# Kernel tuning notes

Hardware: AMD Instinct MI355X
Metric: run time of the kernel (lower is better)

Reference implementation:

```python
import jax, jax.numpy as jnp
import numpy as np

N_NODES = 100000
N_EDGES = 1600000
IN_DIM, HID_DIM, OUT_DIM = 128, 64, 64


def setup_inputs() -> dict:
    key = jax.random.key(0)
    ks = jax.random.split(key, 7)
    x = jax.random.normal(ks[0], (N_NODES, IN_DIM), dtype=jnp.float32)
    edge_index = jax.random.randint(ks[1], (2, N_EDGES), 0, N_NODES, dtype=jnp.int64)
    user_idx = jax.random.randint(ks[2], (N_NODES,), 0, N_NODES, dtype=jnp.int64)
    W1 = jax.random.normal(ks[3], (IN_DIM, HID_DIM), dtype=jnp.float32) * (1.0 / np.sqrt(IN_DIM))
    b1 = jax.random.normal(ks[4], (HID_DIM,), dtype=jnp.float32) * 0.02
    W2 = jax.random.normal(ks[5], (HID_DIM, OUT_DIM), dtype=jnp.float32) * (1.0 / np.sqrt(HID_DIM))
    b2 = jax.random.normal(ks[6], (OUT_DIM,), dtype=jnp.float32) * 0.02
    return {"x": x, "edge_index": edge_index, "user_idx": user_idx,
            "W1": W1, "b1": b1, "W2": W2, "b2": b2}


def _gcn_conv(x, edge_index, W, b):
    # PyG GCNConv: linear transform, add self-loops, sym-normalized aggregation.
    N = x.shape[0]
    h = x @ W  # [N, F_out]
    loop = jnp.arange(N, dtype=edge_index.dtype)
    src = jnp.concatenate([edge_index[0], loop])  # [E+N]
    dst = jnp.concatenate([edge_index[1], loop])
    deg = jax.ops.segment_sum(jnp.ones(src.shape[0], dtype=h.dtype), dst, num_segments=N)
    dis = jnp.where(deg > 0, jax.lax.rsqrt(jnp.maximum(deg, 1.0)), 0.0)  # deg^{-1/2}
    norm = dis[src] * dis[dst]  # [E+N]
    msg = h[src] * norm[:, None]  # gather + scale
    out = jax.ops.segment_sum(msg, dst, num_segments=N)  # scatter-add at targets
    return out + b


def _scatter_mean(x, idx, dim_size):
    s = jax.ops.segment_sum(x, idx, num_segments=dim_size)
    cnt = jax.ops.segment_sum(jnp.ones(x.shape[0], dtype=x.dtype), idx, num_segments=dim_size)
    return jnp.where(cnt[:, None] > 0, s / jnp.maximum(cnt[:, None], 1.0), 0.0)


def reference(x, edge_index, user_idx, W1, b1, W2, b2):
    h = _gcn_conv(x, edge_index, W1, b1)
    h = jax.nn.relu(h)
    # dropout is identity in eval mode
    h = _gcn_conv(h, edge_index, W2, b2)
    return _scatter_mean(h, user_idx, h.shape[0])
```

## Files before the change

### kernel.cpp

```cpp
#include <hip/hip_runtime.h>
#include <hip/hip_bf16.h>


#define FEAT 64
#define INDIM 128

#define SCAN_BS 256
#define SCAN_ELEMS 8
#define SCAN_CHUNK (SCAN_BS * SCAN_ELEMS)

#define BIN_SHIFT 9
#define BIN_R 512
#define BIN_TILE 2048
#define BH_TILE 2048

typedef __attribute__((ext_vector_type(8))) short short8;
typedef __attribute__((ext_vector_type(4))) float f32x4;

__device__ __forceinline__ unsigned short f2bf(float f) {
    unsigned u = __float_as_uint(f);
    unsigned r = u + 0x7FFFu + ((u >> 16) & 1u);
    return (unsigned short)(r >> 16);
}
__device__ __forceinline__ float bf2f(unsigned short v) {
    return __uint_as_float(((unsigned)v) << 16);
}


__global__ __launch_bounds__(256) void k_bhist(const int* __restrict__ dst,
                                               int* __restrict__ gbc,
                                               const int* __restrict__ uidx,
                                               float* __restrict__ cntf,
                                               uint4* __restrict__ outz, long nz4,
                                               int E, int N, int KB) {
    __shared__ int h[256];
    const int tid = threadIdx.x;
    h[tid] = 0;
    __syncthreads();
    const int base = blockIdx.x * BH_TILE;
    #pragma unroll
    for (int t = 0; t < BH_TILE / 256; ++t) {
        int e = base + t * 256 + tid;
        if (e < E) {
            int d = dst[e];
            if ((unsigned)d < (unsigned)N) atomicAdd(&h[d >> BIN_SHIFT], 1);
        }
    }
    int i = blockIdx.x * 256 + tid;
    if (i < N) {
        int u = uidx[i];
        if ((unsigned)u < (unsigned)N) atomicAdd(&cntf[u], 1.0f);
    }
    if (outz) {
        uint4 z; z.x = 0; z.y = 0; z.z = 0; z.w = 0;
        const long stride = (long)gridDim.x * 256;
        for (long idx = (long)blockIdx.x * 256 + tid; idx < nz4; idx += stride)
            outz[idx] = z;
    }
    __syncthreads();
    if (tid < KB && h[tid]) atomicAdd(&gbc[tid], h[tid]);
}

__global__ __launch_bounds__(256) void k_bscan(const int* __restrict__ gbc,
                                               int* __restrict__ bb,
                                               int* __restrict__ bcur,
                                               int* __restrict__ rpN, int KB) {
    __shared__ int lds[256];
    const int tid = threadIdx.x;
    int v = (tid < KB) ? gbc[tid] : 0;
    lds[tid] = v;
    __syncthreads();
    for (int d = 1; d < 256; d <<= 1) {
        int t = (tid >= d) ? lds[tid - d] : 0;
        __syncthreads();
        lds[tid] += t;
        __syncthreads();
    }
    int excl = lds[tid] - v;
    if (tid < KB) { bb[tid] = excl; bcur[tid] = excl; }
    if (tid == 255) { bb[KB] = lds[255]; *rpN = lds[255]; }
}

__global__ __launch_bounds__(256) void k_binA(const int* __restrict__ src,
                                              const int* __restrict__ dst,
                                              int* __restrict__ bcur,
                                              unsigned* __restrict__ pairs,
                                              int E, int N, int KB) {
    __shared__ unsigned lbuf[BIN_TILE];
    __shared__ unsigned short bkt[BIN_TILE];
    __shared__ int lcnt[256];
    __shared__ int loff[256];
    __shared__ int lbase[256];
    __shared__ int tot;
    const int tid = threadIdx.x;
    const int base = blockIdx.x * BIN_TILE;

    lcnt[tid] = 0;
    __syncthreads();

    int mys[BIN_TILE / 256], myd[BIN_TILE / 256], myb[BIN_TILE / 256];
    #pragma unroll
    for (int t = 0; t < BIN_TILE / 256; ++t) {
        int e = base + t * 256 + tid;
        int s = 0, d = -1;
        if (e < E) { s = src[e]; d = dst[e]; }
        if ((unsigned)d >= (unsigned)N) d = -1;
        if ((unsigned)s >= (unsigned)N) s = 0;
        mys[t] = s; myd[t] = d;
        myb[t] = (d >= 0) ? (d >> BIN_SHIFT) : -1;
        if (myb[t] >= 0) atomicAdd(&lcnt[myb[t]], 1);
    }
    __syncthreads();

    int v = lcnt[tid];
    loff[tid] = v;
    __syncthreads();
    for (int d = 1; d < 256; d <<= 1) {
        int t2 = (tid >= d) ? loff[tid - d] : 0;
        __syncthreads();
        loff[tid] += t2;
        __syncthreads();
    }
    if (tid == 255) tot = loff[255];
    int excl = loff[tid] - v;
    __syncthreads();
    loff[tid] = excl;
    lcnt[tid] = excl;
    if (tid < KB && v > 0) lbase[tid] = atomicAdd(&bcur[tid], v);
    __syncthreads();

    #pragma unroll
    for (int t = 0; t < BIN_TILE / 256; ++t) {
        if (myb[t] >= 0) {
            int pos = atomicAdd(&lcnt[myb[t]], 1);
            lbuf[pos] = ((unsigned)mys[t] << BIN_SHIFT) | (unsigned)(myd[t] & (BIN_R - 1));
            bkt[pos] = (unsigned short)myb[t];
        }
    }
    __syncthreads();

    const int T = tot;
    for (int i = tid; i < T; i += 256) {
        int b = bkt[i];
        pairs[lbase[b] + (i - loff[b])] = lbuf[i];
    }
}

__global__ __launch_bounds__(1024) void k_binB2(const unsigned* __restrict__ pairs,
                                                const int* __restrict__ bb,
                                                int* __restrict__ rp,
                                                int* __restrict__ col,
                                                float* __restrict__ dis, int N) {
    __shared__ int cnt[BIN_R];
    __shared__ int cur[BIN_R];
    __shared__ int ssum[256];
    const int tid = threadIdx.x;
    const int b = blockIdx.x;
    const int n0 = b << BIN_SHIFT;
    const int n1 = min(n0 + BIN_R, N);
    const int nn = n1 - n0;
    const int e0 = bb[b];
    const int e1 = bb[b + 1];

    for (int i = tid; i < nn; i += 1024) cnt[i] = 0;
    __syncthreads();
    for (int i = e0 + tid; i < e1; i += 1024) {
        atomicAdd(&cnt[pairs[i] & (BIN_R - 1)], 1);
    }
    __syncthreads();

    const int i0 = 2 * tid;
    int c0 = 0, c1 = 0;
    if (tid < 256) {
        c0 = (i0     < nn) ? cnt[i0]     : 0;
        c1 = (i0 + 1 < nn) ? cnt[i0 + 1] : 0;
        ssum[tid] = c0 + c1;
    }
    __syncthreads();
    for (int d = 1; d < 256; d <<= 1) {
        int t = 0;
        if (tid < 256 && tid >= d) t = ssum[tid - d];
        __syncthreads();
        if (tid < 256) ssum[tid] += t;
        __syncthreads();
    }
    if (tid < 256) {
        int excl = ssum[tid] - (c0 + c1);
        if (i0 < nn) {
            cur[i0] = e0 + excl;
            rp[n0 + i0] = e0 + excl;
            dis[n0 + i0] = rsqrtf((float)c0 + 1.0f);
        }
        if (i0 + 1 < nn) {
            cur[i0 + 1] = e0 + excl + c0;
            rp[n0 + i0 + 1] = e0 + excl + c0;
            dis[n0 + i0 + 1] = rsqrtf((float)c1 + 1.0f);
        }
    }
    __syncthreads();

    for (int i = e0 + tid; i < e1; i += 1024) {
        unsigned p = pairs[i];
        int pos = atomicAdd(&cur[p & (BIN_R - 1)], 1);
        col[pos] = (int)(p >> BIN_SHIFT);
    }
}


__global__ __launch_bounds__(256) void k_hist(const int* __restrict__ dst,
                                              int* __restrict__ cntE, int E, int N) {
    int e = blockIdx.x * 256 + threadIdx.x;
    if (e < E) {
        int d = dst[e];
        if ((unsigned)d < (unsigned)N) atomicAdd(&cntE[d], 1);
    }
}
__global__ __launch_bounds__(256) void k_dis(const int* __restrict__ cntE,
                                             float* __restrict__ dis, int N) {
    int i = blockIdx.x * 256 + threadIdx.x;
    if (i < N) dis[i] = rsqrtf((float)cntE[i] + 1.0f);
}
__global__ __launch_bounds__(SCAN_BS) void k_scan1(const int* __restrict__ c,
                                                   int* __restrict__ rp,
                                                   int* __restrict__ ptot, int N) {
    __shared__ int lds[SCAN_BS];
    const int base = blockIdx.x * SCAN_CHUNK;
    const int tb = base + threadIdx.x * SCAN_ELEMS;
    int vals[SCAN_ELEMS];
    int s = 0;
    #pragma unroll
    for (int k = 0; k < SCAN_ELEMS; ++k) {
        int idx = tb + k;
        int v = (idx < N) ? c[idx] : 0;
        vals[k] = s;
        s += v;
    }
    lds[threadIdx.x] = s;
    __syncthreads();
    for (int d = 1; d < SCAN_BS; d <<= 1) {
        int v = (threadIdx.x >= d) ? lds[threadIdx.x - d] : 0;
        __syncthreads();
        lds[threadIdx.x] += v;
        __syncthreads();
    }
    int toff = (threadIdx.x == 0) ? 0 : lds[threadIdx.x - 1];
    #pragma unroll
    for (int k = 0; k < SCAN_ELEMS; ++k) {
        int idx = tb + k;
        if (idx < N) rp[idx] = toff + vals[k];
    }
    if (threadIdx.x == SCAN_BS - 1) ptot[blockIdx.x] = lds[SCAN_BS - 1];
}
__global__ __launch_bounds__(1024) void k_scan2(int* __restrict__ ptot,
                                                int* __restrict__ poff,
                                                int* __restrict__ rpN, int nb) {
    __shared__ int lds[1024];
    int tid = threadIdx.x;
    lds[tid] = (tid < nb) ? ptot[tid] : 0;
    __syncthreads();
    for (int d = 1; d < 1024; d <<= 1) {
        int v = (tid >= d) ? lds[tid - d] : 0;
        __syncthreads();
        lds[tid] += v;
        __syncthreads();
    }
    if (tid < nb) poff[tid] = (tid == 0) ? 0 : lds[tid - 1];
    if (tid == nb - 1) *rpN = lds[tid];
}
__global__ __launch_bounds__(SCAN_BS) void k_scan3(int* __restrict__ rp,
                                                   const int* __restrict__ poff, int N) {
    int off = poff[blockIdx.x];
    const int tb = blockIdx.x * SCAN_CHUNK + threadIdx.x * SCAN_ELEMS;
    #pragma unroll
    for (int k = 0; k < SCAN_ELEMS; ++k) {
        int idx = tb + k;
        if (idx < N) rp[idx] += off;
    }
}
__global__ __launch_bounds__(256) void k_fill(const int* __restrict__ src,
                                              const int* __restrict__ dst,
                                              const int* __restrict__ rp,
                                              int* __restrict__ tmp,
                                              int* __restrict__ col, int E, int N) {
    int e = blockIdx.x * 256 + threadIdx.x;
    if (e >= E) return;
    int s = src[e], d = dst[e];
    if ((unsigned)s >= (unsigned)N) s = 0;
    if ((unsigned)d >= (unsigned)N) return;
    int r = atomicAdd(&tmp[d], 1);
    col[rp[d] + r] = s;
}

__global__ __launch_bounds__(256) void k_ucnt(const int* __restrict__ uidx,
                                              float* __restrict__ cntf, int N) {
    int i = blockIdx.x * 256 + threadIdx.x;
    if (i < N) {
        int u = uidx[i];
        if ((unsigned)u < (unsigned)N) atomicAdd(&cntf[u], 1.0f);
    }
}


__global__ __launch_bounds__(256) void k_gemm1(const float* __restrict__ x,
                                               const float* __restrict__ W,
                                               const float* __restrict__ scale,
                                               unsigned short* __restrict__ out, int N) {
    __shared__ short wf[4 * 4 * 64 * 8];
    const int tid = threadIdx.x;
    if (blockIdx.x == 0 && tid < 8) {
        uint4 z; z.x = 0; z.y = 0; z.z = 0; z.w = 0;
        *reinterpret_cast<uint4*>(out + (long)N * FEAT + tid * 8) = z;
    }
    for (int i = tid; i < INDIM * FEAT; i += 256) {
        int k = i >> 6, n = i & 63;
        int ct = n >> 4, kc = k >> 5, r = k & 31;
        int owner = ((r >> 3) << 4) | (n & 15);
        wf[(((ct << 2) | kc) * 64 + owner) * 8 + (r & 7)] = (short)f2bf(W[i]);
    }
    __syncthreads();

    const int lane = tid & 63;
    const int m = lane & 15, q = lane >> 4;
    const int row0 = blockIdx.x * 64 + (tid >> 6) * 16;

    short8 bfr[4][4];
    #pragma unroll
    for (int ct = 0; ct < 4; ++ct)
        #pragma unroll
        for (int kc = 0; kc < 4; ++kc)
            bfr[ct][kc] = *reinterpret_cast<const short8*>(&wf[(((ct << 2) | kc) * 64 + lane) * 8]);

    int gr = row0 + m;
    int rl = gr < N ? gr : (N - 1);
    const float* xp = x + (long)rl * INDIM + q * 8;

    f32x4 acc[4] = {{0,0,0,0},{0,0,0,0},{0,0,0,0},{0,0,0,0}};
    #pragma unroll
    for (int kc = 0; kc < 4; ++kc) {
        float4 v0 = *reinterpret_cast<const float4*>(xp + kc * 32);
        float4 v1 = *reinterpret_cast<const float4*>(xp + kc * 32 + 4);
        short8 a;
        a[0]=(short)f2bf(v0.x); a[1]=(short)f2bf(v0.y); a[2]=(short)f2bf(v0.z); a[3]=(short)f2bf(v0.w);
        a[4]=(short)f2bf(v1.x); a[5]=(short)f2bf(v1.y); a[6]=(short)f2bf(v1.z); a[7]=(short)f2bf(v1.w);
        #pragma unroll
        for (int ct = 0; ct < 4; ++ct)
            acc[ct] = __builtin_amdgcn_mfma_f32_16x16x32_bf16(a, bfr[ct][kc], acc[ct], 0, 0, 0);
    }

    #pragma unroll
    for (int reg = 0; reg < 4; ++reg) {
        int row = row0 + q * 4 + reg;
        if (row < N) {
            float sc = scale[row];
            #pragma unroll
            for (int ct = 0; ct < 4; ++ct)
                out[(long)row * FEAT + ct * 16 + m] = f2bf(acc[ct][reg] * sc);
        }
    }
}

__global__ __launch_bounds__(256) void k_gemm2(const unsigned short* __restrict__ h,
                                               const float* __restrict__ W,
                                               const float* __restrict__ scale,
                                               unsigned short* __restrict__ out, int N) {
    __shared__ short wf[4 * 2 * 64 * 8];
    const int tid = threadIdx.x;
    if (blockIdx.x == 0 && tid < 8) {
        uint4 z; z.x = 0; z.y = 0; z.z = 0; z.w = 0;
        *reinterpret_cast<uint4*>(out + (long)N * FEAT + tid * 8) = z;
    }
    for (int i = tid; i < FEAT * FEAT; i += 256) {
        int k = i >> 6, n = i & 63;
        int ct = n >> 4, kc = k >> 5, r = k & 31;
        int owner = ((r >> 3) << 4) | (n & 15);
        wf[(((ct << 1) | kc) * 64 + owner) * 8 + (r & 7)] = (short)f2bf(W[i]);
    }
    __syncthreads();

    const int lane = tid & 63;
    const int m = lane & 15, q = lane >> 4;
    const int row0 = blockIdx.x * 64 + (tid >> 6) * 16;

    short8 bfr[4][2];
    #pragma unroll
    for (int ct = 0; ct < 4; ++ct)
        #pragma unroll
        for (int kc = 0; kc < 2; ++kc)
            bfr[ct][kc] = *reinterpret_cast<const short8*>(&wf[(((ct << 1) | kc) * 64 + lane) * 8]);

    int gr = row0 + m;
    int rl = gr < N ? gr : (N - 1);
    const unsigned short* hp = h + (long)rl * FEAT + q * 8;

    f32x4 acc[4] = {{0,0,0,0},{0,0,0,0},{0,0,0,0},{0,0,0,0}};
    #pragma unroll
    for (int kc = 0; kc < 2; ++kc) {
        short8 a = *reinterpret_cast<const short8*>(hp + kc * 32);
        #pragma unroll
        for (int ct = 0; ct < 4; ++ct)
            acc[ct] = __builtin_amdgcn_mfma_f32_16x16x32_bf16(a, bfr[ct][kc], acc[ct], 0, 0, 0);
    }

    #pragma unroll
    for (int reg = 0; reg < 4; ++reg) {
        int row = row0 + q * 4 + reg;
        if (row < N) {
            float sc = scale[row];
            #pragma unroll
            for (int ct = 0; ct < 4; ++ct)
                out[(long)row * FEAT + ct * 16 + m] = f2bf(acc[ct][reg] * sc);
        }
    }
}


#define ACC8(r)                                                                  \
    a0 += bf2f((unsigned short)(r).x);                                           \
    a1 += bf2f((unsigned short)((r).x >> 16));                                   \
    a2 += bf2f((unsigned short)(r).y);                                           \
    a3 += bf2f((unsigned short)((r).y >> 16));                                   \
    a4 += bf2f((unsigned short)(r).z);                                           \
    a5 += bf2f((unsigned short)((r).z >> 16));                                   \
    a6 += bf2f((unsigned short)(r).w);                                           \
    a7 += bf2f((unsigned short)((r).w >> 16));

#define AGG_BODY(SELF_INIT)                                                      \
    const int lane = threadIdx.x & 63;                                           \
    const int wv = threadIdx.x >> 6;                                             \
    const int p  = lane >> 4;                                                    \
    const int s  = (lane >> 3) & 1;                                              \
    const int ol = lane & 7;                                                     \
    const int i  = blockIdx.x * 16 + wv * 4 + p;                                 \
    const bool valid = (i < N);                                                  \
    const int jb = valid ? rp[i] : 0;                                            \
    const int je = valid ? rp[i + 1] : 0;                                        \
    float a0=0.f,a1=0.f,a2=0.f,a3=0.f,a4=0.f,a5=0.f,a6=0.f,a7=0.f;               \
    if (valid && s == 0) { SELF_INIT }                                           \
    for (int j0 = jb; j0 < je; j0 += 16) {                                       \
        int j1 = j0 + s;                                                         \
        int c1 = (j1      < je) ? col[j1]      : N;                              \
        int c2 = (j1 + 2  < je) ? col[j1 + 2]  : N;                              \
        int c3 = (j1 + 4  < je) ? col[j1 + 4]  : N;                              \
        int c4 = (j1 + 6  < je) ? col[j1 + 6]  : N;                              \
        int c5 = (j1 + 8  < je) ? col[j1 + 8]  : N;                              \
        int c6 = (j1 + 10 < je) ? col[j1 + 10] : N;                              \
        int c7 = (j1 + 12 < je) ? col[j1 + 12] : N;                              \
        int c8 = (j1 + 14 < je) ? col[j1 + 14] : N;                              \
        uint4 r1 = *reinterpret_cast<const uint4*>(A + (long)c1 * FEAT + 8 * ol);\
        uint4 r2 = *reinterpret_cast<const uint4*>(A + (long)c2 * FEAT + 8 * ol);\
        uint4 r3 = *reinterpret_cast<const uint4*>(A + (long)c3 * FEAT + 8 * ol);\
        uint4 r4 = *reinterpret_cast<const uint4*>(A + (long)c4 * FEAT + 8 * ol);\
        uint4 r5 = *reinterpret_cast<const uint4*>(A + (long)c5 * FEAT + 8 * ol);\
        uint4 r6 = *reinterpret_cast<const uint4*>(A + (long)c6 * FEAT + 8 * ol);\
        uint4 r7 = *reinterpret_cast<const uint4*>(A + (long)c7 * FEAT + 8 * ol);\
        uint4 r8 = *reinterpret_cast<const uint4*>(A + (long)c8 * FEAT + 8 * ol);\
        ACC8(r1)                                                                 \
        ACC8(r2)                                                                 \
        ACC8(r3)                                                                 \
        ACC8(r4)                                                                 \
        ACC8(r5)                                                                 \
        ACC8(r6)                                                                 \
        ACC8(r7)                                                                 \
        ACC8(r8)                                                                 \
    }                                                                            \
    a0 += __shfl_xor(a0, 8);  a1 += __shfl_xor(a1, 8);                           \
    a2 += __shfl_xor(a2, 8);  a3 += __shfl_xor(a3, 8);                           \
    a4 += __shfl_xor(a4, 8);  a5 += __shfl_xor(a5, 8);                           \
    a6 += __shfl_xor(a6, 8);  a7 += __shfl_xor(a7, 8);

__global__ __launch_bounds__(256) void k_agg1(const unsigned short* __restrict__ A,
                                              const int* __restrict__ rp,
                                              const int* __restrict__ col,
                                              const float* __restrict__ dis,
                                              const float* __restrict__ bias,
                                              unsigned short* __restrict__ H, int N) {
    AGG_BODY(
        uint4 rv = *reinterpret_cast<const uint4*>(A + (long)i * FEAT + 8 * ol);
        a0 = bf2f((unsigned short)rv.x); a1 = bf2f((unsigned short)(rv.x >> 16));
        a2 = bf2f((unsigned short)rv.y); a3 = bf2f((unsigned short)(rv.y >> 16));
        a4 = bf2f((unsigned short)rv.z); a5 = bf2f((unsigned short)(rv.z >> 16));
        a6 = bf2f((unsigned short)rv.w); a7 = bf2f((unsigned short)(rv.w >> 16));
    )
    if (s == 0 && valid) {
        float di = dis[i];
        float4 b4a = *reinterpret_cast<const float4*>(bias + 8 * ol);
        float4 b4b = *reinterpret_cast<const float4*>(bias + 8 * ol + 4);
        uint4 o;
        o.x = (unsigned)f2bf(fmaxf(fmaf(di, a0, b4a.x), 0.f))
            | ((unsigned)f2bf(fmaxf(fmaf(di, a1, b4a.y), 0.f)) << 16);
        o.y = (unsigned)f2bf(fmaxf(fmaf(di, a2, b4a.z), 0.f))
            | ((unsigned)f2bf(fmaxf(fmaf(di, a3, b4a.w), 0.f)) << 16);
        o.z = (unsigned)f2bf(fmaxf(fmaf(di, a4, b4b.x), 0.f))
            | ((unsigned)f2bf(fmaxf(fmaf(di, a5, b4b.y), 0.f)) << 16);
        o.w = (unsigned)f2bf(fmaxf(fmaf(di, a6, b4b.z), 0.f))
            | ((unsigned)f2bf(fmaxf(fmaf(di, a7, b4b.w), 0.f)) << 16);
        *reinterpret_cast<uint4*>(H + (long)i * FEAT + 8 * ol) = o;
    }
}

__global__ __launch_bounds__(256) void k_agg1f(const unsigned short* __restrict__ A,
                                               const int* __restrict__ rp,
                                               const int* __restrict__ col,
                                               const float* __restrict__ dis,
                                               const float* __restrict__ bias,
                                               const float* __restrict__ W2,
                                               unsigned short* __restrict__ A2, int N) {
    __shared__ short wf[4 * 2 * 64 * 8];
    __shared__ unsigned short hh[16][72];
    __shared__ float dl[16];
    const int tid = threadIdx.x;
    for (int ii = tid; ii < FEAT * FEAT; ii += 256) {
        int k = ii >> 6, n = ii & 63;
        int ct = n >> 4, kc = k >> 5, r = k & 31;
        int owner = ((r >> 3) << 4) | (n & 15);
        wf[(((ct << 1) | kc) * 64 + owner) * 8 + (r & 7)] = (short)f2bf(W2[ii]);
    }
    const int base16 = blockIdx.x * 16;
    if (tid < 16) {
        int node = base16 + tid;
        dl[tid] = (node < N) ? dis[node] : 0.f;
    }
    if (blockIdx.x == 0 && tid >= 32 && tid < 40) {
        uint4 z; z.x = 0; z.y = 0; z.z = 0; z.w = 0;
        *reinterpret_cast<uint4*>(A2 + (long)N * FEAT + (tid - 32) * 8) = z;
    }

    AGG_BODY(
        uint4 rv = *reinterpret_cast<const uint4*>(A + (long)i * FEAT + 8 * ol);
        a0 = bf2f((unsigned short)rv.x); a1 = bf2f((unsigned short)(rv.x >> 16));
        a2 = bf2f((unsigned short)rv.y); a3 = bf2f((unsigned short)(rv.y >> 16));
        a4 = bf2f((unsigned short)rv.z); a5 = bf2f((unsigned short)(rv.z >> 16));
        a6 = bf2f((unsigned short)rv.w); a7 = bf2f((unsigned short)(rv.w >> 16));
    )
    if (s == 0 && valid) {
        float di = dis[i];
        float4 b4a = *reinterpret_cast<const float4*>(bias + 8 * ol);
        float4 b4b = *reinterpret_cast<const float4*>(bias + 8 * ol + 4);
        uint4 o;
        o.x = (unsigned)f2bf(fmaxf(fmaf(di, a0, b4a.x), 0.f))
            | ((unsigned)f2bf(fmaxf(fmaf(di, a1, b4a.y), 0.f)) << 16);
        o.y = (unsigned)f2bf(fmaxf(fmaf(di, a2, b4a.z), 0.f))
            | ((unsigned)f2bf(fmaxf(fmaf(di, a3, b4a.w), 0.f)) << 16);
        o.z = (unsigned)f2bf(fmaxf(fmaf(di, a4, b4b.x), 0.f))
            | ((unsigned)f2bf(fmaxf(fmaf(di, a5, b4b.y), 0.f)) << 16);
        o.w = (unsigned)f2bf(fmaxf(fmaf(di, a6, b4b.z), 0.f))
            | ((unsigned)f2bf(fmaxf(fmaf(di, a7, b4b.w), 0.f)) << 16);
        *reinterpret_cast<uint4*>(&hh[wv * 4 + p][8 * ol]) = o;
    }
    __syncthreads();

    const int m = lane & 15, q = lane >> 4;
    short8 af0 = *reinterpret_cast<const short8*>(&hh[m][q * 8]);
    short8 af1 = *reinterpret_cast<const short8*>(&hh[m][32 + q * 8]);
    short8 bf0 = *reinterpret_cast<const short8*>(&wf[(((wv << 1) | 0) * 64 + lane) * 8]);
    short8 bf1 = *reinterpret_cast<const short8*>(&wf[(((wv << 1) | 1) * 64 + lane) * 8]);
    f32x4 acc = {0, 0, 0, 0};
    acc = __builtin_amdgcn_mfma_f32_16x16x32_bf16(af0, bf0, acc, 0, 0, 0);
    acc = __builtin_amdgcn_mfma_f32_16x16x32_bf16(af1, bf1, acc, 0, 0, 0);
    #pragma unroll
    for (int reg = 0; reg < 4; ++reg) {
        int node = q * 4 + reg;
        int row = base16 + node;
        if (row < N)
            A2[(long)row * FEAT + wv * 16 + m] = f2bf(acc[reg] * dl[node]);
    }
}

__global__ __launch_bounds__(256) void k_agg2s(const unsigned short* __restrict__ A,
                                               const int* __restrict__ rp,
                                               const int* __restrict__ col,
                                               const float* __restrict__ dis,
                                               const float* __restrict__ bias,
                                               const int* __restrict__ uidx,
                                               const float* __restrict__ cntf,
                                               float* __restrict__ S, int N) {
    __shared__ float sbuf[4][4][65];
    AGG_BODY(
        uint4 rv = *reinterpret_cast<const uint4*>(A + (long)i * FEAT + 8 * ol);
        a0 = bf2f((unsigned short)rv.x); a1 = bf2f((unsigned short)(rv.x >> 16));
        a2 = bf2f((unsigned short)rv.y); a3 = bf2f((unsigned short)(rv.y >> 16));
        a4 = bf2f((unsigned short)rv.z); a5 = bf2f((unsigned short)(rv.z >> 16));
        a6 = bf2f((unsigned short)rv.w); a7 = bf2f((unsigned short)(rv.w >> 16));
    )
    if (s == 0) {
        float* dst = &sbuf[wv][p][8 * ol];
        dst[0] = a0; dst[1] = a1; dst[2] = a2; dst[3] = a3;
        dst[4] = a4; dst[5] = a5; dst[6] = a6; dst[7] = a7;
    }
    __syncthreads();
    const int base4 = blockIdx.x * 16 + wv * 4;
    const float bl = bias[lane];
    #pragma unroll
    for (int pp = 0; pp < 4; ++pp) {
        int node = base4 + pp;
        if (node < N) {
            int u = uidx[node];
            if ((unsigned)u < (unsigned)N) {
                float c = cntf[u];
                float wgt = (c > 0.f) ? (1.0f / c) : 0.f;
                float di = dis[node];
                float v = sbuf[wv][pp][lane];
                atomicAdd(&S[(long)u * FEAT + lane], wgt * fmaf(di, v, bl));
            }
        }
    }
}

extern "C" void kernel_launch(void* const* d_in, const int* in_sizes, int n_in,
                              void* d_out, int out_size, void* d_ws, size_t ws_size,
                              hipStream_t stream) {
    const float* x   = (const float*)d_in[0];
    const int* edge  = (const int*)d_in[1];
    const int* uidx  = (const int*)d_in[2];
    const float* W1  = (const float*)d_in[3];
    const float* b1  = (const float*)d_in[4];
    const float* W2  = (const float*)d_in[5];
    const float* b2  = (const float*)d_in[6];
    float* out       = (float*)d_out;

    const int N = in_sizes[2];
    const int E = in_sizes[1] / 2;
    const int* src = edge;
    const int* dst = edge + E;

    const size_t fbuf = (size_t)N * FEAT * sizeof(float);
    const size_t abuf = (size_t)(N + 1) * FEAT * sizeof(unsigned short);
    const int gE   = (E + 255) / 256;
    const int gN   = (N + 255) / 256;
    const int gN16 = (N + 15) / 16;
    const int gG   = (N + 63) / 64;
    const int gBH  = (E + BH_TILE - 1) / BH_TILE;
    const int nbScan = (N + SCAN_CHUNK - 1) / SCAN_CHUNK;
    const int KB = (N + BIN_R - 1) >> BIN_SHIFT;

    auto align256 = [](size_t v) { return (v + 255) & ~(size_t)255; };

    char* w = (char*)d_ws;
    size_t o = 0;
    float* dis  = (float*)(w + o); o = align256(o + (size_t)N * 4);
    float* cntf = (float*)(w + o); o = align256(o + (size_t)N * 4);
    int*   cntE = (int*)  (w + o); o = align256(o + (size_t)N * 4);
    int*   rp   = (int*)  (w + o); o = align256(o + (size_t)(N + 1) * 4);
    int*   ptot = (int*)  (w + o); o = align256(o + (size_t)1024 * 4);
    int*   poff = (int*)  (w + o); o = align256(o + (size_t)1024 * 4);
    int*   col  = (int*)  (w + o); o = align256(o + (size_t)E * 4);
    size_t apsz = (size_t)E * 4 > abuf ? (size_t)E * 4 : abuf;
    char*  Ap   = w + o;           o = align256(o + apsz);
    const size_t need_base = o;
    unsigned short* A2 = (unsigned short*)(w + o); o = align256(o + abuf);
    const size_t need_fused = o;

    int* gbc  = cntE;
    int* bb   = ptot;
    int* bcur = poff;
    unsigned* pairs = (unsigned*)Ap;
    unsigned short* A = (unsigned short*)Ap;
    unsigned short* Hb = (unsigned short*)out;

    const bool binOK = (KB <= 256) && (N <= (1 << (32 - BIN_SHIFT - 1)));
    const long NF4 = (long)N * FEAT / 4;

    if (ws_size >= need_fused && binOK) {
        size_t zspan = (size_t)((char*)gbc - (char*)cntf) + (size_t)KB * 4;
        hipMemsetAsync(cntf, 0, zspan, stream);
        k_bhist<<<gBH, 256, 0, stream>>>(dst, gbc, uidx, cntf,
                                         (uint4*)out, NF4, E, N, KB);
        k_bscan<<<1, 256, 0, stream>>>(gbc, bb, bcur, rp + N, KB);
        k_binA <<<(E + BIN_TILE - 1) / BIN_TILE, 256, 0, stream>>>(src, dst, bcur, pairs, E, N, KB);
        k_binB2<<<KB, 1024, 0, stream>>>(pairs, bb, rp, col, dis, N);

        k_gemm1<<<gG, 256, 0, stream>>>(x, W1, dis, A, N);
        k_agg1f<<<gN16, 256, 0, stream>>>(A, rp, col, dis, b1, W2, A2, N);
        k_agg2s<<<gN16, 256, 0, stream>>>(A2, rp, col, dis, b2, uidx, cntf, out, N);
    } else if (ws_size >= need_base && binOK) {
        size_t zspan = (size_t)((char*)gbc - (char*)cntf) + (size_t)KB * 4;
        hipMemsetAsync(cntf, 0, zspan, stream);
        k_bhist<<<gBH, 256, 0, stream>>>(dst, gbc, uidx, cntf,
                                         (uint4*)nullptr, 0, E, N, KB);
        k_bscan<<<1, 256, 0, stream>>>(gbc, bb, bcur, rp + N, KB);
        k_binA <<<(E + BIN_TILE - 1) / BIN_TILE, 256, 0, stream>>>(src, dst, bcur, pairs, E, N, KB);
        k_binB2<<<KB, 1024, 0, stream>>>(pairs, bb, rp, col, dis, N);

        k_gemm1<<<gG, 256, 0, stream>>>(x, W1, dis, A, N);
        k_agg1 <<<gN16, 256, 0, stream>>>(A, rp, col, dis, b1, Hb, N);
        k_gemm2<<<gG, 256, 0, stream>>>(Hb, W2, dis, A, N);
        hipMemsetAsync(out, 0, fbuf, stream);
        k_agg2s<<<gN16, 256, 0, stream>>>(A, rp, col, dis, b2, uidx, cntf, out, N);
    } else {
        hipMemsetAsync(cntE, 0, (size_t)N * 4, stream);
        k_hist <<<gE, 256, 0, stream>>>(dst, cntE, E, N);
        k_dis  <<<gN, 256, 0, stream>>>(cntE, dis, N);
        k_scan1<<<nbScan, SCAN_BS, 0, stream>>>(cntE, rp, ptot, N);
        k_scan2<<<1, 1024, 0, stream>>>(ptot, poff, rp + N, nbScan);
        k_scan3<<<nbScan, SCAN_BS, 0, stream>>>(rp, poff, N);
        hipMemsetAsync(cntE, 0, (size_t)N * 4, stream);
        k_fill <<<gE, 256, 0, stream>>>(src, dst, rp, cntE, col, E, N);
        hipMemsetAsync(cntf, 0, (size_t)N * 4, stream);
        k_ucnt <<<gN, 256, 0, stream>>>(uidx, cntf, N);
        k_gemm1<<<gG, 256, 0, stream>>>(x, W1, dis, A, N);
        k_agg1 <<<gN16, 256, 0, stream>>>(A, rp, col, dis, b1, Hb, N);
        k_gemm2<<<gG, 256, 0, stream>>>(Hb, W2, dis, A, N);
        hipMemsetAsync(out, 0, fbuf, stream);
        k_agg2s<<<gN16, 256, 0, stream>>>(A, rp, col, dis, b2, uidx, cntf, out, N);
    }
}
```

Measured before the change: 259.2 us.

## Fuse bucket scan into histogram and first GEMM into CSR build kernel

The single-block bucket scan is folded into the histogram kernel through a last-block-done atomic counter, which removes one launch. The first-layer x@W1 MFMA GEMM, with its deg^-1/2 scaling, is moved into the per-bin CSR build kernel, so each 512-node bin also produces its bf16 transformed rows and the separate gemm1 launch disappears. In exchange, the KB (about 196) large blocks now also carry the GEMM, which limits parallelism for that work. Each block also converts all of W1 into LDS, adding redundant work.

```diff
diff --git a/kernel.cpp b/kernel.cpp
--- a/kernel.cpp
+++ b/kernel.cpp
@@ -27,13 +27,18 @@
 }
 
 
-__global__ __launch_bounds__(256) void k_bhist(const int* __restrict__ dst,
-                                               int* __restrict__ gbc,
-                                               const int* __restrict__ uidx,
-                                               float* __restrict__ cntf,
-                                               uint4* __restrict__ outz, long nz4,
-                                               int E, int N, int KB) {
+__global__ __launch_bounds__(256) void k_bhist2(const int* __restrict__ dst,
+                                                int* __restrict__ gbc,
+                                                const int* __restrict__ uidx,
+                                                float* __restrict__ cntf,
+                                                uint4* __restrict__ outz, long nz4,
+                                                unsigned* __restrict__ done,
+                                                int* __restrict__ bb,
+                                                int* __restrict__ bcur,
+                                                int* __restrict__ rpN,
+                                                int E, int N, int KB) {
     __shared__ int h[256];
+    __shared__ int isLast;
     const int tid = threadIdx.x;
     h[tid] = 0;
     __syncthreads();
@@ -59,26 +64,28 @@
     }
     __syncthreads();
     if (tid < KB && h[tid]) atomicAdd(&gbc[tid], h[tid]);
-}
-
-__global__ __launch_bounds__(256) void k_bscan(const int* __restrict__ gbc,
-                                               int* __restrict__ bb,
-                                               int* __restrict__ bcur,
-                                               int* __restrict__ rpN, int KB) {
-    __shared__ int lds[256];
-    const int tid = threadIdx.x;
-    int v = (tid < KB) ? gbc[tid] : 0;
-    lds[tid] = v;
-    __syncthreads();
-    for (int d = 1; d < 256; d <<= 1) {
-        int t = (tid >= d) ? lds[tid - d] : 0;
-        __syncthreads();
-        lds[tid] += t;
-        __syncthreads();
-    }
-    int excl = lds[tid] - v;
-    if (tid < KB) { bb[tid] = excl; bcur[tid] = excl; }
-    if (tid == 255) { bb[KB] = lds[255]; *rpN = lds[255]; }
+    __threadfence();
+    __syncthreads();
+    if (tid == 0) {
+        unsigned t = atomicAdd(done, 1u);
+        isLast = (t == (unsigned)(gridDim.x - 1));
+    }
+    __syncthreads();
+    if (isLast) {
+        __threadfence();
+        int v = (tid < KB) ? atomicAdd(&gbc[tid], 0) : 0;
+        h[tid] = v;
+        __syncthreads();
+        for (int d = 1; d < 256; d <<= 1) {
+            int t2 = (tid >= d) ? h[tid - d] : 0;
+            __syncthreads();
+            h[tid] += t2;
+            __syncthreads();
+        }
+        int excl = h[tid] - v;
+        if (tid < KB) { bb[tid] = excl; bcur[tid] = excl; }
+        if (tid == 255) { bb[KB] = h[255]; *rpN = h[255]; }
+    }
 }
 
 __global__ __launch_bounds__(256) void k_binA(const int* __restrict__ src,
@@ -143,6 +150,118 @@
     for (int i = tid; i < T; i += 256) {
         int b = bkt[i];
         pairs[lbase[b] + (i - loff[b])] = lbuf[i];
+    }
+}
+
+__global__ __launch_bounds__(1024) void k_binB2g(const unsigned* __restrict__ pairs,
+                                                 const int* __restrict__ bb,
+                                                 int* __restrict__ rp,
+                                                 int* __restrict__ col,
+                                                 float* __restrict__ dis,
+                                                 const float* __restrict__ x,
+                                                 const float* __restrict__ W1,
+                                                 unsigned short* __restrict__ A, int N) {
+    __shared__ int cnt[BIN_R];
+    __shared__ int cur[BIN_R];
+    __shared__ int ssum[256];
+    __shared__ short wf[4 * 4 * 64 * 8];
+    const int tid = threadIdx.x;
+    const int b = blockIdx.x;
+    const int n0 = b << BIN_SHIFT;
+    const int n1 = min(n0 + BIN_R, N);
+    const int nn = n1 - n0;
+    const int e0 = bb[b];
+    const int e1 = bb[b + 1];
+
+    for (int ii = tid; ii < INDIM * FEAT; ii += 1024) {
+        int k = ii >> 6, n = ii & 63;
+        int ct = n >> 4, kc = k >> 5, r = k & 31;
+        int owner = ((r >> 3) << 4) | (n & 15);
+        wf[(((ct << 2) | kc) * 64 + owner) * 8 + (r & 7)] = (short)f2bf(W1[ii]);
+    }
+    if (b == 0 && tid >= 512 && tid < 520) {
+        uint4 z; z.x = 0; z.y = 0; z.z = 0; z.w = 0;
+        *reinterpret_cast<uint4*>(A + (long)N * FEAT + (tid - 512) * 8) = z;
+    }
+
+    for (int i = tid; i < nn; i += 1024) cnt[i] = 0;
+    __syncthreads();
+    for (int i = e0 + tid; i < e1; i += 1024) {
+        atomicAdd(&cnt[pairs[i] & (BIN_R - 1)], 1);
+    }
+    __syncthreads();
+
+    const int i0 = 2 * tid;
+    int c0 = 0, c1 = 0;
+    if (tid < 256) {
+        c0 = (i0     < nn) ? cnt[i0]     : 0;
+        c1 = (i0 + 1 < nn) ? cnt[i0 + 1] : 0;
+        ssum[tid] = c0 + c1;
+    }
+    __syncthreads();
+    for (int d = 1; d < 256; d <<= 1) {
+        int t = 0;
+        if (tid < 256 && tid >= d) t = ssum[tid - d];
+        __syncthreads();
+        if (tid < 256) ssum[tid] += t;
+        __syncthreads();
+    }
+    if (tid < 256) {
+        int excl = ssum[tid] - (c0 + c1);
+        if (i0 < nn) {
+            cur[i0] = e0 + excl;
+            rp[n0 + i0] = e0 + excl;
+            dis[n0 + i0] = rsqrtf((float)c0 + 1.0f);
+        }
+        if (i0 + 1 < nn) {
+            cur[i0 + 1] = e0 + excl + c0;
+            rp[n0 + i0 + 1] = e0 + excl + c0;
+            dis[n0 + i0 + 1] = rsqrtf((float)c1 + 1.0f);
+        }
+    }
+    __syncthreads();
+
+    for (int i = e0 + tid; i < e1; i += 1024) {
+        unsigned p = pairs[i];
+        int pos = atomicAdd(&cur[p & (BIN_R - 1)], 1);
+        col[pos] = (int)(p >> BIN_SHIFT);
+    }
+    __syncthreads();
+
+    const int lane = tid & 63;
+    const int w = tid >> 6;
+    const int m = lane & 15, q = lane >> 4;
+    #pragma unroll
+    for (int t = 0; t < 2; ++t) {
+        int lrow = w * 32 + t * 16 + m;
+        int gr = n0 + lrow;
+        int rl = gr < N ? gr : (N - 1);
+        const float* xp = x + (long)rl * INDIM + q * 8;
+        f32x4 acc[4] = {{0,0,0,0},{0,0,0,0},{0,0,0,0},{0,0,0,0}};
+        #pragma unroll
+        for (int kc = 0; kc < 4; ++kc) {
+            float4 v0 = *reinterpret_cast<const float4*>(xp + kc * 32);
+            float4 v1 = *reinterpret_cast<const float4*>(xp + kc * 32 + 4);
+            short8 a;
+            a[0]=(short)f2bf(v0.x); a[1]=(short)f2bf(v0.y); a[2]=(short)f2bf(v0.z); a[3]=(short)f2bf(v0.w);
+            a[4]=(short)f2bf(v1.x); a[5]=(short)f2bf(v1.y); a[6]=(short)f2bf(v1.z); a[7]=(short)f2bf(v1.w);
+            #pragma unroll
+            for (int ct = 0; ct < 4; ++ct) {
+                short8 bf = *reinterpret_cast<const short8*>(&wf[(((ct << 2) | kc) * 64 + lane) * 8]);
+                acc[ct] = __builtin_amdgcn_mfma_f32_16x16x32_bf16(a, bf, acc[ct], 0, 0, 0);
+            }
+        }
+        #pragma unroll
+        for (int reg = 0; reg < 4; ++reg) {
+            int ld = w * 32 + t * 16 + q * 4 + reg;
+            if (ld < nn) {
+                float sc = rsqrtf((float)cnt[ld] + 1.0f);
+                int row = n0 + ld;
+                #pragma unroll
+                for (int ct = 0; ct < 4; ++ct)
+                    A[(long)row * FEAT + ct * 16 + m] = f2bf(acc[ct][reg] * sc);
+            }
+        }
     }
 }
 
@@ -583,9 +702,9 @@
         a6 = bf2f((unsigned short)rv.w); a7 = bf2f((unsigned short)(rv.w >> 16));
     )
     if (s == 0) {
-        float* dst = &sbuf[wv][p][8 * ol];
-        dst[0] = a0; dst[1] = a1; dst[2] = a2; dst[3] = a3;
-        dst[4] = a4; dst[5] = a5; dst[6] = a6; dst[7] = a7;
+        float* dl = &sbuf[wv][p][8 * ol];
+        dl[0] = a0; dl[1] = a1; dl[2] = a2; dl[3] = a3;
+        dl[4] = a4; dl[5] = a5; dl[6] = a6; dl[7] = a7;
     }
     __syncthreads();
     const int base4 = blockIdx.x * 16 + wv * 4;
@@ -647,45 +766,43 @@
     size_t apsz = (size_t)E * 4 > abuf ? (size_t)E * 4 : abuf;
     char*  Ap   = w + o;           o = align256(o + apsz);
     const size_t need_base = o;
-    unsigned short* A2 = (unsigned short*)(w + o); o = align256(o + abuf);
+    unsigned short* Asep = (unsigned short*)(w + o); o = align256(o + abuf);
     const size_t need_fused = o;
 
     int* gbc  = cntE;
+    unsigned* done = (unsigned*)(gbc + KB);
     int* bb   = ptot;
     int* bcur = poff;
     unsigned* pairs = (unsigned*)Ap;
-    unsigned short* A = (unsigned short*)Ap;
+    unsigned short* A2t1 = (unsigned short*)Ap;
+    unsigned short* At2  = (unsigned short*)Ap;
     unsigned short* Hb = (unsigned short*)out;
 
-    const bool binOK = (KB <= 256) && (N <= (1 << (32 - BIN_SHIFT - 1)));
+    const bool binOK = (KB <= 256) && (N <= (1 << (32 - BIN_SHIFT - 1))) && (KB + 1 <= N);
     const long NF4 = (long)N * FEAT / 4;
 
     if (ws_size >= need_fused && binOK) {
-        size_t zspan = (size_t)((char*)gbc - (char*)cntf) + (size_t)KB * 4;
+        size_t zspan = (size_t)((char*)gbc - (char*)cntf) + (size_t)(KB + 1) * 4;
         hipMemsetAsync(cntf, 0, zspan, stream);
-        k_bhist<<<gBH, 256, 0, stream>>>(dst, gbc, uidx, cntf,
-                                         (uint4*)out, NF4, E, N, KB);
-        k_bscan<<<1, 256, 0, stream>>>(gbc, bb, bcur, rp + N, KB);
+        k_bhist2<<<gBH, 256, 0, stream>>>(dst, gbc, uidx, cntf, (uint4*)out, NF4,
+                                          done, bb, bcur, rp + N, E, N, KB);
+        k_binA  <<<(E + BIN_TILE - 1) / BIN_TILE, 256, 0, stream>>>(src, dst, bcur, pairs, E, N, KB);
+        k_binB2g<<<KB, 1024, 0, stream>>>(pairs, bb, rp, col, dis, x, W1, Asep, N);
+        k_agg1f <<<gN16, 256, 0, stream>>>(Asep, rp, col, dis, b1, W2, A2t1, N);
+        k_agg2s <<<gN16, 256, 0, stream>>>(A2t1, rp, col, dis, b2, uidx, cntf, out, N);
+    } else if (ws_size >= need_base && binOK) {
+        size_t zspan = (size_t)((char*)gbc - (char*)cntf) + (size_t)(KB + 1) * 4;
+        hipMemsetAsync(cntf, 0, zspan, stream);
+        k_bhist2<<<gBH, 256, 0, stream>>>(dst, gbc, uidx, cntf, (uint4*)nullptr, 0,
+                                          done, bb, bcur, rp + N, E, N, KB);
         k_binA <<<(E + BIN_TILE - 1) / BIN_TILE, 256, 0, stream>>>(src, dst, bcur, pairs, E, N, KB);
         k_binB2<<<KB, 1024, 0, stream>>>(pairs, bb, rp, col, dis, N);
 
-        k_gemm1<<<gG, 256, 0, stream>>>(x, W1, dis, A, N);
-        k_agg1f<<<gN16, 256, 0, stream>>>(A, rp, col, dis, b1, W2, A2, N);
-        k_agg2s<<<gN16, 256, 0, stream>>>(A2, rp, col, dis, b2, uidx, cntf, out, N);
-    } else if (ws_size >= need_base && binOK) {
-        size_t zspan = (size_t)((char*)gbc - (char*)cntf) + (size_t)KB * 4;
-        hipMemsetAsync(cntf, 0, zspan, stream);
-        k_bhist<<<gBH, 256, 0, stream>>>(dst, gbc, uidx, cntf,
-                                         (uint4*)nullptr, 0, E, N, KB);
-        k_bscan<<<1, 256, 0, stream>>>(gbc, bb, bcur, rp + N, KB);
-        k_binA <<<(E + BIN_TILE - 1) / BIN_TILE, 256, 0, stream>>>(src, dst, bcur, pairs, E, N, KB);
-        k_binB2<<<KB, 1024, 0, stream>>>(pairs, bb, rp, col, dis, N);
-
-        k_gemm1<<<gG, 256, 0, stream>>>(x, W1, dis, A, N);
-        k_agg1 <<<gN16, 256, 0, stream>>>(A, rp, col, dis, b1, Hb, N);
-        k_gemm2<<<gG, 256, 0, stream>>>(Hb, W2, dis, A, N);
+        k_gemm1<<<gG, 256, 0, stream>>>(x, W1, dis, At2, N);
+        k_agg1 <<<gN16, 256, 0, stream>>>(At2, rp, col, dis, b1, Hb, N);
+        k_gemm2<<<gG, 256, 0, stream>>>(Hb, W2, dis, At2, N);
         hipMemsetAsync(out, 0, fbuf, stream);
-        k_agg2s<<<gN16, 256, 0, stream>>>(A, rp, col, dis, b2, uidx, cntf, out, N);
+        k_agg2s<<<gN16, 256, 0, stream>>>(At2, rp, col, dis, b2, uidx, cntf, out, N);
     } else {
         hipMemsetAsync(cntE, 0, (size_t)N * 4, stream);
         k_hist <<<gE, 256, 0, stream>>>(dst, cntE, E, N);
@@ -697,10 +814,10 @@
         k_fill <<<gE, 256, 0, stream>>>(src, dst, rp, cntE, col, E, N);
         hipMemsetAsync(cntf, 0, (size_t)N * 4, stream);
         k_ucnt <<<gN, 256, 0, stream>>>(uidx, cntf, N);
-        k_gemm1<<<gG, 256, 0, stream>>>(x, W1, dis, A, N);
-        k_agg1 <<<gN16, 256, 0, stream>>>(A, rp, col, dis, b1, Hb, N);
-        k_gemm2<<<gG, 256, 0, stream>>>(Hb, W2, dis, A, N);
+        k_gemm1<<<gG, 256, 0, stream>>>(x, W1, dis, At2, N);
+        k_agg1 <<<gN16, 256, 0, stream>>>(At2, rp, col, dis, b1, Hb, N);
+        k_gemm2<<<gG, 256, 0, stream>>>(Hb, W2, dis, At2, N);
         hipMemsetAsync(out, 0, fbuf, stream);
-        k_agg2s<<<gN16, 256, 0, stream>>>(A, rp, col, dis, b2, uidx, cntf, out, N);
-    }
-}
+        k_agg2s<<<gN16, 256, 0, stream>>>(At2, rp, col, dis, b2, uidx, cntf, out, N);
+    }
+}
```

New measurement: 327.9 us. +26.5%, slower.
